# Performance work log

Hardware: AMD Instinct MI355X
Metric: run time of the kernel (lower is better)

## Reference

```python
import jax, jax.numpy as jnp
import numpy as np

N = 50000
E = 800000
IN_FEATS = 128
OUT_FEATS = 64
HEADS = 4
NEG_SLOPE = 0.2  # DGL GATConv default


def _glorot(key, shape):
    fan_in, fan_out = shape[0], shape[-1]
    lim = jnp.sqrt(6.0 / (fan_in + fan_out))
    return jax.random.uniform(key, shape, jnp.float32, -lim, lim)


def setup_inputs() -> dict:
    key = jax.random.key(0)
    ks = jax.random.split(key, 16)
    D = OUT_FEATS // HEADS  # per-head dim of layers 0..num_layers-2
    inp = {
        "h": jax.random.normal(ks[0], (N, IN_FEATS), jnp.float32),
        "src": jax.random.randint(ks[1], (E,), 0, N, jnp.int32),
        "dst": jax.random.randint(ks[2], (E,), 0, N, jnp.int32),
        # layer 0: in_feats -> heads x D
        "W0": _glorot(ks[3], (IN_FEATS, HEADS * D)),
        "al0": _glorot(ks[4], (HEADS, D)),
        "ar0": _glorot(ks[5], (HEADS, D)),
        "b0": jnp.zeros((HEADS * D,), jnp.float32),
        # layer 1: heads*D -> heads x D
        "W1": _glorot(ks[6], (HEADS * D, HEADS * D)),
        "al1": _glorot(ks[7], (HEADS, D)),
        "ar1": _glorot(ks[8], (HEADS, D)),
        "b1": jnp.zeros((HEADS * D,), jnp.float32),
        "W2": _glorot(ks[9], (HEADS * D, OUT_FEATS)),
        "al2": _glorot(ks[10], (1, OUT_FEATS)),
        "ar2": _glorot(ks[11], (1, OUT_FEATS)),
        "b2": jnp.zeros((OUT_FEATS,), jnp.float32),
    }
    return inp


def gat_conv(h, W, al, ar, b, src, dst):
    """DGL GATConv (shared src/dst features, allow_zero_in_degree).
    h: [N, F_in]; W: [F_in, H*D]; al, ar: [H, D]; b: [H*D].
    Returns [N, H, D].
    """
    H, D = al.shape
    f = (h @ W).reshape(-1, H, D)                 # [N, H, D]
    el = jnp.einsum("nhd,hd->nh", f, al)          # [N, H]
    er = jnp.einsum("nhd,hd->nh", f, ar)          # [N, H]
    e = jax.nn.leaky_relu(el[src] + er[dst], NEG_SLOPE)  # [E, H]
    # segment softmax over incoming edges of each dst node
    m = jax.ops.segment_max(e, dst, num_segments=N)      # [N, H]
    ex = jnp.exp(e - m[dst])                              # [E, H]
    s = jax.ops.segment_sum(ex, dst, num_segments=N)      # [N, H]
    a = ex / s[dst]                                       # [E, H]
    msg = a[:, :, None] * f[src]                          # [E, H, D]
    out = jax.ops.segment_sum(msg, dst, num_segments=N)   # [N, H, D]
    return out + b.reshape(1, H, D)


def reference(h, src, dst, W0, al0, ar0, b0, W1, al1, ar1, b1, W2, al2, ar2, b2):
    x = gat_conv(h, W0, al0, ar0, b0, src, dst).reshape(N, -1)
    x = jax.nn.elu(x)
    x = gat_conv(x, W1, al1, ar1, b1, src, dst).reshape(N, -1)
    x = jax.nn.elu(x)
    x = gat_conv(x, W2, al2, ar2, b2, src, dst)  # [N, 1, OUT_FEATS]
    return jnp.squeeze(x, axis=1)                # [N, OUT_FEATS]
```

## Files before the change

### kernel.cpp

```cpp
#include <hip/hip_runtime.h>
#include <hip/hip_bf16.h>

typedef unsigned short u16;
typedef unsigned int   u32;
typedef __attribute__((ext_vector_type(2))) float f32x2;

__device__ __forceinline__ float bf2f(u32 bits) { return __uint_as_float(bits << 16); }
__device__ __forceinline__ u32 f2bf_bits(float x) {
    u32 u = __float_as_uint(x);
    return (u + 0x7fffu + ((u >> 16) & 1u)) >> 16;
}
__device__ __forceinline__ float exp2_raw(float x) {
    float r; asm("v_exp_f32 %0, %1" : "=v"(r) : "v"(x)); return r;
}

__global__ __launch_bounds__(256) void cvt_zero_det(
    const u32* __restrict__ hw,
    const void* __restrict__ W0, const void* __restrict__ al0, const void* __restrict__ ar0, const void* __restrict__ b0,
    const void* __restrict__ W1, const void* __restrict__ al1, const void* __restrict__ ar1, const void* __restrict__ b1,
    const void* __restrict__ W2, const void* __restrict__ al2, const void* __restrict__ ar2, const void* __restrict__ b2,
    float* __restrict__ P, int* __restrict__ flag, int* __restrict__ deg, int NP)
{
    int t = threadIdx.x;
    int gstr = gridDim.x * 256;
    for (int z = blockIdx.x * 256 + t; z < NP; z += gstr) deg[z] = 0;

    if (blockIdx.x >= 67) return;

    __shared__ int s_hit;
    if (t == 0) s_hit = 0;
    __syncthreads();
    int hit = 0;
    for (int i = t; i < 8192; i += 256) {
        u32 lo = hw[i] & 0xffffu;
        if (((lo >> 7) & 0xffu) == 0xffu) hit = 1;
    }
    if (hit) atomicOr(&s_hit, 1);
    __syncthreads();
    int f32in = s_hit;
    if (blockIdx.x == 0 && t == 0) *flag = f32in;

    int i = blockIdx.x * 256 + t;
    const void* s; int off;
    if      (i < 8192)  { s = W0;  off = 0;     }
    else if (i < 12288) { s = W1;  off = 8192;  }
    else if (i < 16384) { s = W2;  off = 12288; }
    else if (i < 16448) { s = al0; off = 16384; }
    else if (i < 16512) { s = ar0; off = 16448; }
    else if (i < 16576) { s = b0;  off = 16512; }
    else if (i < 16640) { s = al1; off = 16576; }
    else if (i < 16704) { s = ar1; off = 16640; }
    else if (i < 16768) { s = b1;  off = 16704; }
    else if (i < 16832) { s = al2; off = 16768; }
    else if (i < 16896) { s = ar2; off = 16832; }
    else if (i < 16960) { s = b2;  off = 16896; }
    else return;
    int j = i - off;
    float v = f32in ? ((const float*)s)[j] : bf2f(((const u16*)s)[j]);
    bool is_attn = (i >= 16384) && !((i >= 16512 && i < 16576) ||
                                     (i >= 16704 && i < 16768) ||
                                     (i >= 16896));
    if (is_attn) v *= 1.44269504088896340736f;
    P[i] = v;
}

__global__ __launch_bounds__(256) void hist_rank(
    const int* __restrict__ dst, int* __restrict__ deg, int* __restrict__ rank, int E)
{
    int e = blockIdx.x * 256 + threadIdx.x;
    if (e < E) rank[e] = atomicAdd(&deg[dst[e]], 1);
}

__global__ __launch_bounds__(256) void scan_all(
    const int* __restrict__ deg, int* __restrict__ row_start)
{
    __shared__ int sm[256];
    int t = threadIdx.x;
    int c = blockIdx.x;

    int pre = 0;
    int nInt4 = c * 256;
    const int4* dp = (const int4*)deg;
    for (int j = t; j < nInt4; j += 256) {
        int4 v = dp[j];
        pre += v.x + v.y + v.z + v.w;
    }
    sm[t] = pre;
    __syncthreads();
#pragma unroll
    for (int off = 128; off; off >>= 1) {
        if (t < off) sm[t] += sm[t + off];
        __syncthreads();
    }
    int base = sm[0];
    __syncthreads();

    size_t boff = (size_t)c * 1024;
    int4 v = ((const int4*)(deg + boff))[t];
    int tsum = v.x + v.y + v.z + v.w;
    sm[t] = tsum;
    __syncthreads();
#pragma unroll
    for (int off = 1; off < 256; off <<= 1) {
        int a = (t >= off) ? sm[t - off] : 0;
        __syncthreads();
        sm[t] += a;
        __syncthreads();
    }
    int excl = sm[t] - tsum + base;
    int4 r;
    r.x = excl;
    r.y = excl + v.x;
    r.z = excl + v.x + v.y;
    r.w = excl + v.x + v.y + v.z;
    ((int4*)(row_start + boff))[t] = r;
}

__global__ __launch_bounds__(256) void scatter_kernel(
    const int* __restrict__ src, const int* __restrict__ dst, const int* __restrict__ rank,
    const int* __restrict__ row_start, int* __restrict__ csr_src, int E)
{
    int e = blockIdx.x * 256 + threadIdx.x;
    if (e < E) csr_src[row_start[dst[e]] + rank[e]] = src[e];
}

template<int F_IN, int H, bool LAYER0>
__global__ __launch_bounds__(256) void gemm_attn(
    const int* __restrict__ flag, const void* __restrict__ xv,
    const float* __restrict__ Wf, const float* __restrict__ alf, const float* __restrict__ arf,
    u16* __restrict__ fo, float* __restrict__ el, float* __restrict__ er, int N)
{
    int lane = threadIdx.x & 63;
    int cg   = __builtin_amdgcn_readfirstlane(threadIdx.x >> 6);
    int n    = blockIdx.x * 64 + lane;
    bool act = (n < N);

    float acc[16];
#pragma unroll
    for (int c = 0; c < 16; c++) acc[c] = 0.f;

    const float* Wcol = Wf + cg * 16;
    bool f32in = LAYER0 ? (*flag != 0) : false;

    if (act) {
        if (f32in) {
            const float* x = (const float*)xv + (size_t)n * F_IN;
            for (int k0 = 0; k0 < F_IN; k0 += 4) {
                float4 u = *reinterpret_cast<const float4*>(x + k0);
                float xs[4] = {u.x, u.y, u.z, u.w};
#pragma unroll
                for (int j = 0; j < 4; j++) {
                    const float* w = Wcol + (size_t)(k0 + j) * 64;
#pragma unroll
                    for (int c = 0; c < 16; c++) acc[c] = fmaf(xs[j], w[c], acc[c]);
                }
            }
        } else {
            const u16* x = (const u16*)xv + (size_t)n * F_IN;
            for (int k0 = 0; k0 < F_IN; k0 += 8) {
                uint4 u = *reinterpret_cast<const uint4*>(x + k0);
                float xs[8];
                xs[0] = bf2f(u.x & 0xffffu); xs[1] = bf2f(u.x >> 16);
                xs[2] = bf2f(u.y & 0xffffu); xs[3] = bf2f(u.y >> 16);
                xs[4] = bf2f(u.z & 0xffffu); xs[5] = bf2f(u.z >> 16);
                xs[6] = bf2f(u.w & 0xffffu); xs[7] = bf2f(u.w >> 16);
#pragma unroll
                for (int j = 0; j < 8; j++) {
                    const float* w = Wcol + (size_t)(k0 + j) * 64;
#pragma unroll
                    for (int c = 0; c < 16; c++) acc[c] = fmaf(xs[j], w[c], acc[c]);
                }
            }
        }
    }

    float e1 = 0.f, e2 = 0.f;
#pragma unroll
    for (int c = 0; c < 16; c++) {
        e1 = fmaf(acc[c], alf[cg * 16 + c], e1);
        e2 = fmaf(acc[c], arf[cg * 16 + c], e2);
    }
    if constexpr (H == 4) {
        if (act) {
            el[(size_t)n * 4 + cg] = e1;
            er[(size_t)n * 4 + cg] = e2;
        }
    } else {
        __shared__ float sel[4][64];
        __shared__ float ser[4][64];
        sel[cg][lane] = e1;
        ser[cg][lane] = e2;
        __syncthreads();
        if (cg == 0 && act) {
            el[n] = sel[0][lane] + sel[1][lane] + sel[2][lane] + sel[3][lane];
            er[n] = ser[0][lane] + ser[1][lane] + ser[2][lane] + ser[3][lane];
        }
    }

    if (act) {
        u16* dp = fo + (size_t)n * 64 + cg * 16;
        uint4 v;
        v.x = f2bf_bits(acc[0])  | (f2bf_bits(acc[1])  << 16);
        v.y = f2bf_bits(acc[2])  | (f2bf_bits(acc[3])  << 16);
        v.z = f2bf_bits(acc[4])  | (f2bf_bits(acc[5])  << 16);
        v.w = f2bf_bits(acc[6])  | (f2bf_bits(acc[7])  << 16);
        *reinterpret_cast<uint4*>(dp) = v;
        v.x = f2bf_bits(acc[8])  | (f2bf_bits(acc[9])  << 16);
        v.y = f2bf_bits(acc[10]) | (f2bf_bits(acc[11]) << 16);
        v.z = f2bf_bits(acc[12]) | (f2bf_bits(acc[13]) << 16);
        v.w = f2bf_bits(acc[14]) | (f2bf_bits(acc[15]) << 16);
        *reinterpret_cast<uint4*>(dp + 8) = v;
    }
}

template<int H, bool FINAL>
__global__ __launch_bounds__(256) void aggregate(
    const int* __restrict__ flag,
    const u16* __restrict__ fo, const float* __restrict__ el, const float* __restrict__ er,
    const int* __restrict__ row_start, const int* __restrict__ csr_src,
    const float* __restrict__ bias, void* __restrict__ outp, int N)
{
    int gid  = blockIdx.x * 256 + threadIdx.x;
    int n    = __builtin_amdgcn_readfirstlane(gid >> 6);
    int lane = threadIdx.x & 63;
    if (n >= N) return;
    constexpr int D = 64 / H;
    int h = lane / D;
    float erh = er[n * H + h];
    int i0 = __builtin_amdgcn_readfirstlane(row_start[n]);
    int i1 = __builtin_amdgcn_readfirstlane(row_start[n + 1]);

    f32x2 erh2 = {erh, erh};
    f32x2 sAcc = {0.f, 0.f};
    f32x2 aAcc = {0.f, 0.f};
    float s0 = 0.f, a0 = 0.f;
    int i = i0;

    for (; i + 8 <= i1; i += 8) {
        int s[8];
#pragma unroll
        for (int j = 0; j < 8; j++) s[j] = __builtin_amdgcn_readfirstlane(csr_src[i + j]);
        float ev[8], fv[8];
#pragma unroll
        for (int j = 0; j < 8; j++) ev[j] = (el + s[j] * H)[h];
#pragma unroll
        for (int j = 0; j < 8; j++) fv[j] = bf2f((fo + ((size_t)s[j] << 6))[lane]);
#pragma unroll
        for (int j = 0; j < 8; j += 2) {
            f32x2 ev2 = {ev[j], ev[j + 1]};
            f32x2 t   = ev2 + erh2;
            f32x2 u   = t * 0.2f;
            float vA = fmaxf(t.x, u.x);
            float vB = fmaxf(t.y, u.y);
            f32x2 ex2 = {exp2_raw(vA), exp2_raw(vB)};
            f32x2 fv2 = {fv[j], fv[j + 1]};
            sAcc += ex2;
            aAcc = ex2 * fv2 + aAcc;
        }
    }
    for (; i + 4 <= i1; i += 4) {
        int s[4];
#pragma unroll
        for (int j = 0; j < 4; j++) s[j] = __builtin_amdgcn_readfirstlane(csr_src[i + j]);
        float ev[4], fv[4];
#pragma unroll
        for (int j = 0; j < 4; j++) ev[j] = (el + s[j] * H)[h];
#pragma unroll
        for (int j = 0; j < 4; j++) fv[j] = bf2f((fo + ((size_t)s[j] << 6))[lane]);
#pragma unroll
        for (int j = 0; j < 4; j += 2) {
            f32x2 ev2 = {ev[j], ev[j + 1]};
            f32x2 t   = ev2 + erh2;
            f32x2 u   = t * 0.2f;
            float vA = fmaxf(t.x, u.x);
            float vB = fmaxf(t.y, u.y);
            f32x2 ex2 = {exp2_raw(vA), exp2_raw(vB)};
            f32x2 fv2 = {fv[j], fv[j + 1]};
            sAcc += ex2;
            aAcc = ex2 * fv2 + aAcc;
        }
    }
    for (; i < i1; i++) {
        int s = __builtin_amdgcn_readfirstlane(csr_src[i]);
        const float* ep = el + s * H;
        float v = ep[h] + erh;
        v = fmaxf(v, 0.2f * v);
        float ex = exp2_raw(v);
        const u16* fp = fo + ((size_t)s << 6);
        float fv = bf2f(fp[lane]);
        s0 += ex;
        a0 = fmaf(ex, fv, a0);
    }

    float sumex = (sAcc.x + sAcc.y) + s0;
    float acc   = (aAcc.x + aAcc.y) + a0;
    float o;
    if (i1 > i0) o = acc * __builtin_amdgcn_rcpf(sumex) + bias[lane];
    else         o = bias[lane];
    size_t idx = (size_t)n * 64 + lane;
    if constexpr (!FINAL) {
        float t = exp2_raw(o * 1.44269504088896340736f);
        o = o > 0.f ? o : (t - 1.f);
        ((u16*)outp)[idx] = f2bf_bits(o);
    } else {
        if (*flag) ((float*)outp)[idx] = o;
        else       ((u16*)outp)[idx]   = f2bf_bits(o);
    }
}

extern "C" void kernel_launch(void* const* d_in, const int* in_sizes, int n_in,
                              void* d_out, int out_size, void* d_ws, size_t ws_size,
                              hipStream_t stream)
{
    const void* h    = d_in[0];
    const int*  srcp = (const int*)d_in[1];
    const int*  dstp = (const int*)d_in[2];

    const int N  = in_sizes[0] / 128;
    const int E  = in_sizes[1];
    const int NP = (N + 1024) & ~1023;
    const int B  = NP / 1024;

    char* ws = (char*)d_ws;
    size_t off = 0;
    auto take = [&](size_t bytes) -> char* {
        char* p = ws + off;
        off = (off + bytes + 255) & ~(size_t)255;
        return p;
    };
    float* P         = (float*)take(16960 * 4);
    int*   flag      = (int*)  take(256);
    float* el        = (float*)take((size_t)N * 4 * 4);
    float* er        = (float*)take((size_t)N * 4 * 4);
    int*   deg       = (int*)  take((size_t)NP * 4);
    int*   row_start = (int*)  take((size_t)NP * 4);
    int*   rank      = (int*)  take((size_t)E * 4);
    int*   csr_src   = (int*)  take((size_t)E * 4);
    u16*   f         = (u16*)  take((size_t)N * 64 * 2);
    u16*   x1        = (u16*)  take((size_t)N * 64 * 2);
    if (off > ws_size) x1 = (u16*)d_out;

    float* Wf0  = P;          float* Wf1  = P + 8192;  float* Wf2  = P + 12288;
    float* alf0 = P + 16384;  float* arf0 = P + 16448; float* bf0  = P + 16512;
    float* alf1 = P + 16576;  float* arf1 = P + 16640; float* bf1  = P + 16704;
    float* alf2 = P + 16768;  float* arf2 = P + 16832; float* bf2  = P + 16896;

    int cz_blocks = (NP + 255) / 256;
    if (cz_blocks < 67) cz_blocks = 67;
    cvt_zero_det<<<cz_blocks, 256, 0, stream>>>((const u32*)h,
        d_in[3], d_in[4], d_in[5], d_in[6],
        d_in[7], d_in[8], d_in[9], d_in[10],
        d_in[11], d_in[12], d_in[13], d_in[14], P, flag, deg, NP);

    hist_rank<<<(E + 255) / 256, 256, 0, stream>>>(dstp, deg, rank, E);
    scan_all<<<B, 256, 0, stream>>>(deg, row_start);
    scatter_kernel<<<(E + 255) / 256, 256, 0, stream>>>(srcp, dstp, rank, row_start, csr_src, E);

    int gemm_blocks = (N + 63) / 64;
    int agg_blocks  = (N * 64 + 255) / 256;

    gemm_attn<128, 4, true ><<<gemm_blocks, 256, 0, stream>>>(flag, h,  Wf0, alf0, arf0, f, el, er, N);
    aggregate<4, false><<<agg_blocks, 256, 0, stream>>>(flag, f, el, er, row_start, csr_src, bf0, x1, N);
    gemm_attn<64, 4, false><<<gemm_blocks, 256, 0, stream>>>(flag, x1, Wf1, alf1, arf1, f, el, er, N);
    aggregate<4, false><<<agg_blocks, 256, 0, stream>>>(flag, f, el, er, row_start, csr_src, bf1, x1, N);
    gemm_attn<64, 1, false><<<gemm_blocks, 256, 0, stream>>>(flag, x1, Wf2, alf2, arf2, f, el, er, N);
    aggregate<1, true ><<<agg_blocks, 256, 0, stream>>>(flag, f, el, er, row_start, csr_src, bf2, d_out, N);
}
```

Measured before the change: 298.5 us.

## Precompute per-edge attention exponentials in a separate kernel before aggregation

Adds an edge_scores kernel that computes leaky-relu and exp2 of el[src]+er[dst] for every edge and writes the result into CSR order. Aggregate then reads these weights contiguously instead of gathering el per source and computing exp inline. The intent is to replace the scattered el gathers and transcendental work in the latency-bound aggregate loop with coalesced loads. The cost is an extra launch per layer and 12.8MB of writes plus reads for H=4, with fallback buffer aliasing when workspace is small, which could be fragile.

Measured after the change: 335.4 us. +12.4%, slower.

```diff
diff --git a/kernel.cpp b/kernel.cpp
--- a/kernel.cpp
+++ b/kernel.cpp
@@ -213,10 +213,34 @@
     }
 }
 
+template<int H>
+__global__ __launch_bounds__(256) void edge_scores(
+    const int* __restrict__ src, const int* __restrict__ dst,
+    const int* __restrict__ rank, const int* __restrict__ row_start,
+    const float* __restrict__ el, const float* __restrict__ er,
+    float* __restrict__ w, int E)
+{
+    int t = blockIdx.x * 256 + threadIdx.x;
+    int e = (H == 4) ? (t >> 2) : t;
+    if (e >= E) return;
+    int s = src[e], d = dst[e];
+    int slot = row_start[d] + rank[e];
+    if constexpr (H == 4) {
+        int h = t & 3;
+        float sc = el[(s << 2) + h] + er[(d << 2) + h];
+        sc = fmaxf(sc, 0.2f * sc);
+        w[(slot << 2) + h] = exp2_raw(sc);
+    } else {
+        float sc = el[s] + er[d];
+        sc = fmaxf(sc, 0.2f * sc);
+        w[slot] = exp2_raw(sc);
+    }
+}
+
 template<int H, bool FINAL>
 __global__ __launch_bounds__(256) void aggregate(
     const int* __restrict__ flag,
-    const u16* __restrict__ fo, const float* __restrict__ el, const float* __restrict__ er,
+    const u16* __restrict__ fo, const float* __restrict__ w,
     const int* __restrict__ row_start, const int* __restrict__ csr_src,
     const float* __restrict__ bias, void* __restrict__ outp, int N)
 {
@@ -226,11 +250,9 @@
     if (n >= N) return;
     constexpr int D = 64 / H;
     int h = lane / D;
-    float erh = er[n * H + h];
     int i0 = __builtin_amdgcn_readfirstlane(row_start[n]);
     int i1 = __builtin_amdgcn_readfirstlane(row_start[n + 1]);
 
-    f32x2 erh2 = {erh, erh};
     f32x2 sAcc = {0.f, 0.f};
     f32x2 aAcc = {0.f, 0.f};
     float s0 = 0.f, a0 = 0.f;
@@ -240,56 +262,44 @@
         int s[8];
 #pragma unroll
         for (int j = 0; j < 8; j++) s[j] = __builtin_amdgcn_readfirstlane(csr_src[i + j]);
-        float ev[8], fv[8];
-#pragma unroll
-        for (int j = 0; j < 8; j++) ev[j] = (el + s[j] * H)[h];
+        float wv[8], fv[8];
+#pragma unroll
+        for (int j = 0; j < 8; j++)
+            wv[j] = (H == 4) ? w[((i + j) << 2) + h] : w[i + j];
 #pragma unroll
         for (int j = 0; j < 8; j++) fv[j] = bf2f((fo + ((size_t)s[j] << 6))[lane]);
 #pragma unroll
         for (int j = 0; j < 8; j += 2) {
-            f32x2 ev2 = {ev[j], ev[j + 1]};
-            f32x2 t   = ev2 + erh2;
-            f32x2 u   = t * 0.2f;
-            float vA = fmaxf(t.x, u.x);
-            float vB = fmaxf(t.y, u.y);
-            f32x2 ex2 = {exp2_raw(vA), exp2_raw(vB)};
-            f32x2 fv2 = {fv[j], fv[j + 1]};
-            sAcc += ex2;
-            aAcc = ex2 * fv2 + aAcc;
+            f32x2 w2 = {wv[j], wv[j + 1]};
+            f32x2 f2 = {fv[j], fv[j + 1]};
+            sAcc += w2;
+            aAcc = w2 * f2 + aAcc;
         }
     }
     for (; i + 4 <= i1; i += 4) {
         int s[4];
 #pragma unroll
         for (int j = 0; j < 4; j++) s[j] = __builtin_amdgcn_readfirstlane(csr_src[i + j]);
-        float ev[4], fv[4];
-#pragma unroll
-        for (int j = 0; j < 4; j++) ev[j] = (el + s[j] * H)[h];
+        float wv[4], fv[4];
+#pragma unroll
+        for (int j = 0; j < 4; j++)
+            wv[j] = (H == 4) ? w[((i + j) << 2) + h] : w[i + j];
 #pragma unroll
         for (int j = 0; j < 4; j++) fv[j] = bf2f((fo + ((size_t)s[j] << 6))[lane]);
 #pragma unroll
         for (int j = 0; j < 4; j += 2) {
-            f32x2 ev2 = {ev[j], ev[j + 1]};
-            f32x2 t   = ev2 + erh2;
-            f32x2 u   = t * 0.2f;
-            float vA = fmaxf(t.x, u.x);
-            float vB = fmaxf(t.y, u.y);
-            f32x2 ex2 = {exp2_raw(vA), exp2_raw(vB)};
-            f32x2 fv2 = {fv[j], fv[j + 1]};
-            sAcc += ex2;
-            aAcc = ex2 * fv2 + aAcc;
+            f32x2 w2 = {wv[j], wv[j + 1]};
+            f32x2 f2 = {fv[j], fv[j + 1]};
+            sAcc += w2;
+            aAcc = w2 * f2 + aAcc;
         }
     }
     for (; i < i1; i++) {
         int s = __builtin_amdgcn_readfirstlane(csr_src[i]);
-        const float* ep = el + s * H;
-        float v = ep[h] + erh;
-        v = fmaxf(v, 0.2f * v);
-        float ex = exp2_raw(v);
-        const u16* fp = fo + ((size_t)s << 6);
-        float fv = bf2f(fp[lane]);
-        s0 += ex;
-        a0 = fmaf(ex, fv, a0);
+        float wvv = (H == 4) ? w[(i << 2) + h] : w[i];
+        float fv = bf2f((fo + ((size_t)s << 6))[lane]);
+        s0 += wvv;
+        a0 = fmaf(wvv, fv, a0);
     }
 
     float sumex = (sAcc.x + sAcc.y) + s0;
@@ -340,6 +350,14 @@
     u16*   x1        = (u16*)  take((size_t)N * 64 * 2);
     if (off > ws_size) x1 = (u16*)d_out;
 
+    size_t off_before_w4 = off;
+    float* w4 = (float*)take((size_t)E * 4 * 4);
+    if (off > ws_size) { w4 = (float*)d_out; off = off_before_w4; }
+    size_t off_before_w1 = off;
+    float* w1 = (float*)take((size_t)E * 4);
+    if (off > ws_size) { w1 = w4; off = off_before_w1; }
+    if (w1 == w4 && (void*)w4 == d_out) w1 = (float*)x1;
+
     float* Wf0  = P;          float* Wf1  = P + 8192;  float* Wf2  = P + 12288;
     float* alf0 = P + 16384;  float* arf0 = P + 16448; float* bf0  = P + 16512;
     float* alf1 = P + 16576;  float* arf1 = P + 16640; float* bf1  = P + 16704;
@@ -358,11 +376,16 @@
 
     int gemm_blocks = (N + 63) / 64;
     int agg_blocks  = (N * 64 + 255) / 256;
+    int sc4_blocks  = (E * 4 + 255) / 256;
+    int sc1_blocks  = (E + 255) / 256;
 
     gemm_attn<128, 4, true ><<<gemm_blocks, 256, 0, stream>>>(flag, h,  Wf0, alf0, arf0, f, el, er, N);
-    aggregate<4, false><<<agg_blocks, 256, 0, stream>>>(flag, f, el, er, row_start, csr_src, bf0, x1, N);
+    edge_scores<4><<<sc4_blocks, 256, 0, stream>>>(srcp, dstp, rank, row_start, el, er, w4, E);
+    aggregate<4, false><<<agg_blocks, 256, 0, stream>>>(flag, f, w4, row_start, csr_src, bf0, x1, N);
     gemm_attn<64, 4, false><<<gemm_blocks, 256, 0, stream>>>(flag, x1, Wf1, alf1, arf1, f, el, er, N);
-    aggregate<4, false><<<agg_blocks, 256, 0, stream>>>(flag, f, el, er, row_start, csr_src, bf1, x1, N);
+    edge_scores<4><<<sc4_blocks, 256, 0, stream>>>(srcp, dstp, rank, row_start, el, er, w4, E);
+    aggregate<4, false><<<agg_blocks, 256, 0, stream>>>(flag, f, w4, row_start, csr_src, bf1, x1, N);
     gemm_attn<64, 1, false><<<gemm_blocks, 256, 0, stream>>>(flag, x1, Wf2, alf2, arf2, f, el, er, N);
-    aggregate<1, true ><<<agg_blocks, 256, 0, stream>>>(flag, f, el, er, row_start, csr_src, bf2, d_out, N);
-}
+    edge_scores<1><<<sc1_blocks, 256, 0, stream>>>(srcp, dstp, rank, row_start, el, er, w1, E);
+    aggregate<1, true ><<<agg_blocks, 256, 0, stream>>>(flag, f, w1, row_start, csr_src, bf2, d_out, N);
+}
```
